# Optimization experiments

Measured on AMD Instinct MI355X. Metric: run time of the kernel, lower is better.

Reference implementation:

```python
import jax, jax.numpy as jnp
import numpy as np

B, T, D, H = 4, 2048, 1024, 16
HD = D // H  # head dim = 64


def setup_inputs() -> dict:
    key = jax.random.key(0)
    ks = jax.random.split(key, 9)
    s_in = 1.0 / np.sqrt(D)
    return {
        "token_embedding": jax.random.normal(ks[0], (B, T, D), dtype=jnp.float32),
        # per-head projections, batched over head axis: [H, D, HD]
        "Wq": jax.random.normal(ks[1], (H, D, HD), dtype=jnp.float32) * s_in,
        "bq": jnp.zeros((H, HD), dtype=jnp.float32),
        "Wk": jax.random.normal(ks[2], (H, D, HD), dtype=jnp.float32) * s_in,
        "bk": jnp.zeros((H, HD), dtype=jnp.float32),
        "Wv": jax.random.normal(ks[3], (H, D, HD), dtype=jnp.float32) * s_in,
        "bv": jnp.zeros((H, HD), dtype=jnp.float32),
        "Wo": jax.random.normal(ks[4], (D, D), dtype=jnp.float32) * s_in,
        "bo": jnp.zeros((D,), dtype=jnp.float32),
    }


def _mha(x, Wq, bq, Wk, bk, Wv, bv, Wo, bo):
    # x: [B,T,D]; per-head proj -> [B,H,T,HD]
    q = jnp.einsum('btd,hde->bhte', x, Wq) + bq[None, :, None, :]
    k = jnp.einsum('btd,hde->bhte', x, Wk) + bk[None, :, None, :]
    v = jnp.einsum('btd,hde->bhte', x, Wv) + bv[None, :, None, :]
    scores = jnp.einsum('bhte,bhse->bhts', q, k) / jnp.sqrt(jnp.float32(HD))
    causal = jnp.tril(jnp.ones((T, T), dtype=bool))
    scores = jnp.where(causal[None, None], scores, jnp.float32(-jnp.inf))
    attn = jax.nn.softmax(scores, axis=-1)
    ctx = jnp.einsum('bhts,bhse->bhte', attn, v)  # [B,H,T,HD]
    # concat heads (head order matches ModuleList order) -> [B,T,D]
    cat = jnp.transpose(ctx, (0, 2, 1, 3)).reshape(B, T, D)
    return cat @ Wo + bo


def reference(token_embedding, Wq, bq, Wk, bk, Wv, bv, Wo, bo):
    return _mha(token_embedding, Wq, bq, Wk, bk, Wv, bv, Wo, bo)
```

## Files before the change

### kernel.cpp

```cpp
#include <hip/hip_runtime.h>
#include <hip/hip_bf16.h>
#include <stdint.h>
#include <stddef.h>

#define B_ 4
#define T_ 2048
#define D_ 1024
#define H_ 16
#define HD_ 64
#define LDQKV (3 * D_)

typedef __attribute__((ext_vector_type(8))) __bf16 bf16x8;
typedef __attribute__((ext_vector_type(4))) float f32x4;
typedef __attribute__((ext_vector_type(16))) float f32x16;

#define AS1V const __attribute__((address_space(1))) void*
#define AS3V __attribute__((address_space(3))) void*

__global__ void prep_kernel(const float* __restrict__ x, const float* __restrict__ Wq,
                            const float* __restrict__ Wk, const float* __restrict__ Wv,
                            const float* __restrict__ Wo, const float* __restrict__ bq,
                            const float* __restrict__ bk, const float* __restrict__ bv,
                            __bf16* __restrict__ xb, __bf16* __restrict__ wT,
                            __bf16* __restrict__ woT, float* __restrict__ bqkv) {
    const int bid = blockIdx.x, tid = threadIdx.x;
    if (bid < 4096) {
        int i = bid * 256 + tid;
        const float4* p = (const float4*)(x + (size_t)i * 8);
        float4 a = p[0], b = p[1];
        bf16x8 o;
        o[0] = (__bf16)a.x; o[1] = (__bf16)a.y; o[2] = (__bf16)a.z; o[3] = (__bf16)a.w;
        o[4] = (__bf16)b.x; o[5] = (__bf16)b.y; o[6] = (__bf16)b.z; o[7] = (__bf16)b.w;
        *(bf16x8*)(xb + (size_t)i * 8) = o;
    } else if (bid < 16384) {
        int wbid = bid - 4096;
        int which = wbid >> 12;
        int rem = wbid & 4095;
        int h = rem >> 8, z = rem & 255;
        const float* W = (which == 0) ? Wq : (which == 1) ? Wk : Wv;
        int e = tid & 63, dd = tid >> 6;
        float v = W[((size_t)h * D_ + z * 4 + dd) * HD_ + e];
        wT[((size_t)which * D_ + h * HD_ + e) * D_ + z * 4 + dd] = (__bf16)v;
    } else if (bid < 17408) {
        int k = bid - 16384;
        for (int n = tid; n < D_; n += 256)
            woT[(size_t)n * D_ + k] = (__bf16)Wo[(size_t)k * D_ + n];
    } else {
        int n = (bid - 17408) * 256 + tid;
        const float* b = (n < D_) ? bq : (n < 2 * D_) ? bk : bv;
        bqkv[n] = b[n & (D_ - 1)];
    }
}

template <typename OutT>
__global__ __launch_bounds__(256, 3)
void gemm_bt_kernel(const __bf16* __restrict__ A, const __bf16* __restrict__ Bt,
                    OutT* __restrict__ C, const float* __restrict__ bias,
                    int M, int N, int K, int lda, int ldb, int ldc) {
    __shared__ __bf16 lsA[128 * 64];
    __shared__ __bf16 lsB[128 * 64];
    const int tid = threadIdx.x;
    const int lane = tid & 63;
    const int wave = tid >> 6;
    const int wr = wave >> 1, wc = wave & 1;
    const int lc = lane & 15, lg = lane >> 4;
    const long row0 = (long)blockIdx.y * 128;
    const long col0 = (long)blockIdx.x * 128;

    f32x4 acc[4][4];
#pragma unroll
    for (int mi = 0; mi < 4; mi++)
#pragma unroll
        for (int ni = 0; ni < 4; ni++)
#pragma unroll
            for (int q = 0; q < 4; q++) acc[mi][ni][q] = 0.f;

    const int s_row = tid >> 3, s_k8 = tid & 7;

    for (int k0 = 0; k0 < K; k0 += 64) {
        __syncthreads();
#pragma unroll
        for (int c2 = 0; c2 < 4; c2++) {
            const __bf16* ga = A + (row0 + c2 * 32 + s_row) * (long)lda + k0 + s_k8 * 8;
            const __bf16* gb = Bt + (col0 + c2 * 32 + s_row) * (long)ldb + k0 + s_k8 * 8;
            __bf16* la = lsA + ((c2 << 8) + (wave << 6)) * 8;
            __bf16* lb = lsB + ((c2 << 8) + (wave << 6)) * 8;
            __builtin_amdgcn_global_load_lds((AS1V)ga, (AS3V)la, 16, 0, 0);
            __builtin_amdgcn_global_load_lds((AS1V)gb, (AS3V)lb, 16, 0, 0);
        }
        __syncthreads();
#pragma unroll
        for (int kk = 0; kk < 2; kk++) {
            bf16x8 af[4], bf_[4];
#pragma unroll
            for (int mi = 0; mi < 4; mi++)
                af[mi] = *(const bf16x8*)(lsA + (wr * 64 + mi * 16 + lc) * 64 + (kk * 4 + lg) * 8);
#pragma unroll
            for (int ni = 0; ni < 4; ni++)
                bf_[ni] = *(const bf16x8*)(lsB + (wc * 64 + ni * 16 + lc) * 64 + (kk * 4 + lg) * 8);
#pragma unroll
            for (int mi = 0; mi < 4; mi++)
#pragma unroll
                for (int ni = 0; ni < 4; ni++)
                    acc[mi][ni] =
                        __builtin_amdgcn_mfma_f32_16x16x32_bf16(af[mi], bf_[ni], acc[mi][ni], 0, 0, 0);
        }
    }

#pragma unroll
    for (int mi = 0; mi < 4; mi++) {
#pragma unroll
        for (int ni = 0; ni < 4; ni++) {
            long r0 = row0 + wr * 64 + mi * 16 + lg * 4;
            long cc = col0 + wc * 64 + ni * 16 + lc;
            float bv = bias[cc];
#pragma unroll
            for (int q = 0; q < 4; q++) {
                float v = acc[mi][ni][q] + bv;
                C[(r0 + q) * (long)ldc + cc] = (OutT)v;
            }
        }
    }
}

__global__ void transpose_v_kernel(const __bf16* __restrict__ qkv, __bf16* __restrict__ vT) {
    __shared__ __bf16 tile[64][72];
    const int bh = blockIdx.y, t0 = blockIdx.x * 64;
    const int b = bh >> 4, h = bh & 15;
    const int r = threadIdx.x >> 2, c16 = (threadIdx.x & 3) * 16;
    const __bf16* src = qkv + (size_t)(b * T_ + t0 + r) * LDQKV + 2 * D_ + h * HD_ + c16;
    *(bf16x8*)&tile[r][c16] = *(const bf16x8*)src;
    *(bf16x8*)&tile[r][c16 + 8] = *(const bf16x8*)(src + 8);
    __syncthreads();
    bf16x8 v0, v1;
#pragma unroll
    for (int j = 0; j < 8; j++) v0[j] = tile[c16 + j][r];
#pragma unroll
    for (int j = 0; j < 8; j++) v1[j] = tile[c16 + 8 + j][r];
    __bf16* dst = vT + (size_t)(bh * HD_ + r) * T_ + t0 + c16;
    *(bf16x8*)dst = v0;
    *(bf16x8*)(dst + 8) = v1;
}

__global__ __launch_bounds__(256, 3)
void attn_kernel(const __bf16* __restrict__ qkv, const __bf16* __restrict__ vT,
                 __bf16* __restrict__ ctx) {
    __shared__ __bf16 lsK[64 * 64];
    __shared__ __bf16 lsV[64 * 64];
    const int tid = threadIdx.x;
    const int lane = tid & 63, w = tid >> 6;
    const int l31 = lane & 31, hi = lane >> 5;
    const int bid = blockIdx.x;
    const int xcd = bid & 7, slot = bid >> 3;
    const int bh = xcd * 8 + (slot & 7);
    const int pr = slot >> 3;
    const int b = bh >> 4, h = bh & 15;
    const float K2 = 0.125f * 1.44269504f;

    const __bf16* kbase = qkv + (size_t)(b * T_) * LDQKV + D_ + h * HD_;
    const __bf16* vbase = vT + (size_t)bh * HD_ * T_;

    int s_row[2], s_ch[2];
#pragma unroll
    for (int c2 = 0; c2 < 2; c2++) {
        int idx = c2 * 256 + tid;
        s_row[c2] = idx >> 3;
        s_ch[c2] = idx & 7;
    }

    for (int phase = 0; phase < 2; ++phase) {
        const int chunk = phase ? pr : (15 - pr);
        const int q0 = chunk * 128;
        const int qw = q0 + w * 32;
        const int myq = qw + l31;

        const __bf16* qbase = qkv + (size_t)(b * T_ + myq) * LDQKV + h * HD_;
        bf16x8 qf[4];
#pragma unroll
        for (int kf = 0; kf < 4; kf++) qf[kf] = *(const bf16x8*)(qbase + kf * 16 + hi * 8);

        f32x16 accO[2];
#pragma unroll
        for (int eo = 0; eo < 2; eo++)
#pragma unroll
            for (int r = 0; r < 16; r++) accO[eo][r] = 0.f;
        float m_r = -1e30f, l_r = 0.f;

        bf16x8 rK[2], rV[2];
        auto loadKV = [&](int kv0) {
#pragma unroll
            for (int c2 = 0; c2 < 2; c2++) {
                rK[c2] = *(const bf16x8*)(kbase + (size_t)(kv0 + s_row[c2]) * LDQKV + s_ch[c2] * 8);
                rV[c2] = *(const bf16x8*)(vbase + (size_t)s_row[c2] * T_ + kv0 + s_ch[c2] * 8);
            }
        };

        const int ntiles = 2 * (chunk + 1);
        loadKV(0);
        for (int it = 0; it < ntiles; ++it) {
            const int kv0 = it << 6;
            __syncthreads();
#pragma unroll
            for (int c2 = 0; c2 < 2; c2++) {
                *(bf16x8*)(lsK + s_row[c2] * 64 + ((s_ch[c2] ^ (s_row[c2] & 7)) << 3)) = rK[c2];
                *(bf16x8*)(lsV + s_row[c2] * 64 + ((s_ch[c2] ^ (s_row[c2] & 7)) << 3)) = rV[c2];
            }
            __syncthreads();
            if (it + 1 < ntiles) loadKV((it + 1) << 6);

            if (kv0 > qw + 31) continue;

            f32x16 st[2];
            __builtin_amdgcn_s_setprio(1);
#pragma unroll
            for (int kh = 0; kh < 2; kh++) {
                f32x16 a;
#pragma unroll
                for (int r = 0; r < 16; r++) a[r] = 0.f;
#pragma unroll
                for (int kf = 0; kf < 4; kf++) {
                    int row = kh * 32 + l31;
                    int ch = (kf << 1) | hi;
                    bf16x8 kfrag = *(const bf16x8*)(lsK + row * 64 + ((ch ^ (row & 7)) << 3));
                    a = __builtin_amdgcn_mfma_f32_32x32x16_bf16(kfrag, qf[kf], a, 0, 0, 0);
                }
                st[kh] = a;
            }
            __builtin_amdgcn_s_setprio(0);

            if (kv0 + 63 > qw) {
                const int qmk = myq - kv0 - 4 * hi;
#pragma unroll
                for (int kh = 0; kh < 2; kh++)
#pragma unroll
                    for (int r = 0; r < 16; r++) {
                        int kvl = (r & 3) + 8 * (r >> 2) + kh * 32;
                        if (kvl > qmk) st[kh][r] = -1e30f;
                    }
            }

            float red[16];
#pragma unroll
            for (int r = 0; r < 16; r++) red[r] = fmaxf(st[0][r], st[1][r]);
#pragma unroll
            for (int s2 = 8; s2 >= 1; s2 >>= 1)
#pragma unroll
                for (int r = 0; r < s2; r++) red[r] = fmaxf(red[r], red[r + s2]);
            float pmax = fmaxf(red[0], __shfl_xor(red[0], 32));

            if (!__all(pmax - m_r <= 64.f)) {
                float m_new = fmaxf(m_r, pmax);
                float alpha = exp2f((m_r - m_new) * K2);
                l_r *= alpha;
#pragma unroll
                for (int eo = 0; eo < 2; eo++)
#pragma unroll
                    for (int r = 0; r < 16; r++) accO[eo][r] *= alpha;
                m_r = m_new;
            }

            const float mb = m_r * K2;
#pragma unroll
            for (int kh = 0; kh < 2; kh++)
#pragma unroll
                for (int r = 0; r < 16; r++) st[kh][r] = exp2f(fmaf(st[kh][r], K2, -mb));

            float sr[16];
#pragma unroll
            for (int r = 0; r < 16; r++) sr[r] = st[0][r] + st[1][r];
#pragma unroll
            for (int s2 = 8; s2 >= 1; s2 >>= 1)
#pragma unroll
                for (int r = 0; r < s2; r++) sr[r] += sr[r + s2];
            l_r += sr[0] + __shfl_xor(sr[0], 32);

            union BW { unsigned u[4]; bf16x8 v; };
            bf16x8 pfrag[4];
            auto pack2 = [](float a, float b) -> unsigned {
                union { __bf16 h[2]; unsigned u; } x;
                x.h[0] = (__bf16)a;
                x.h[1] = (__bf16)b;
                return x.u;
            };
#pragma unroll
            for (int kh = 0; kh < 2; kh++)
#pragma unroll
                for (int sub = 0; sub < 2; sub++) {
                    int base = sub * 8;
                    unsigned W1 = pack2(st[kh][base + 0], st[kh][base + 1]);
                    unsigned W3 = pack2(st[kh][base + 2], st[kh][base + 3]);
                    unsigned W2 = pack2(st[kh][base + 4], st[kh][base + 5]);
                    unsigned W4 = pack2(st[kh][base + 6], st[kh][base + 7]);
                    unsigned X1 = (unsigned)__shfl_xor((int)W1, 32);
                    unsigned X2 = (unsigned)__shfl_xor((int)W2, 32);
                    unsigned X3 = (unsigned)__shfl_xor((int)W3, 32);
                    unsigned X4 = (unsigned)__shfl_xor((int)W4, 32);
                    BW bw;
                    bw.u[0] = hi ? X2 : W1;
                    bw.u[1] = hi ? X4 : W3;
                    bw.u[2] = hi ? W2 : X1;
                    bw.u[3] = hi ? W4 : X3;
                    pfrag[kh * 2 + sub] = bw.v;
                }

            __builtin_amdgcn_s_setprio(1);
#pragma unroll
            for (int eo = 0; eo < 2; eo++) {
#pragma unroll
                for (int ks = 0; ks < 4; ks++) {
                    int row = eo * 32 + l31;
                    int ch = (ks << 1) | hi;
                    bf16x8 vfrag = *(const bf16x8*)(lsV + row * 64 + ((ch ^ (row & 7)) << 3));
                    accO[eo] = __builtin_amdgcn_mfma_f32_32x32x16_bf16(vfrag, pfrag[ks], accO[eo], 0, 0, 0);
                }
            }
            __builtin_amdgcn_s_setprio(0);
        }

        float invl = 1.0f / l_r;
        __bf16* cb = ctx + (size_t)(b * T_ + myq) * D_ + h * HD_;
#pragma unroll
        for (int eo = 0; eo < 2; eo++)
#pragma unroll
            for (int r = 0; r < 16; r++) {
                int e = eo * 32 + (r & 3) + 8 * (r >> 2) + 4 * hi;
                cb[e] = (__bf16)(accO[eo][r] * invl);
            }
    }
}

extern "C" void kernel_launch(void* const* d_in, const int* in_sizes, int n_in,
                              void* d_out, int out_size, void* d_ws, size_t ws_size,
                              hipStream_t stream) {
    const float* x = (const float*)d_in[0];
    const float* Wq = (const float*)d_in[1];
    const float* bq = (const float*)d_in[2];
    const float* Wk = (const float*)d_in[3];
    const float* bk = (const float*)d_in[4];
    const float* Wv = (const float*)d_in[5];
    const float* bv = (const float*)d_in[6];
    const float* Wo = (const float*)d_in[7];
    const float* bo = (const float*)d_in[8];
    float* out = (float*)d_out;

    char* ws = (char*)d_ws;
    size_t off = 0;
    auto alloc = [&](size_t bytes) -> void* {
        off = (off + 255) & ~(size_t)255;
        void* p = ws + off;
        off += bytes;
        return p;
    };
    __bf16* xb = (__bf16*)alloc((size_t)B_ * T_ * D_ * 2);
    __bf16* wT = (__bf16*)alloc((size_t)3 * D_ * D_ * 2);
    float* bqkv = (float*)alloc((size_t)3 * D_ * 4);
    __bf16* woT = (__bf16*)alloc((size_t)D_ * D_ * 2);
    __bf16* qkv = (__bf16*)alloc((size_t)B_ * T_ * 3 * D_ * 2);
    __bf16* vTb = (__bf16*)alloc((size_t)B_ * H_ * HD_ * T_ * 2);
    __bf16* ctx = (__bf16*)alloc((size_t)B_ * T_ * D_ * 2);
    (void)ws_size;
    (void)in_sizes;
    (void)n_in;
    (void)out_size;

    prep_kernel<<<17420, 256, 0, stream>>>(x, Wq, Wk, Wv, Wo, bq, bk, bv, xb, wT, woT, bqkv);

    gemm_bt_kernel<__bf16><<<dim3(3 * D_ / 128, B_ * T_ / 128), 256, 0, stream>>>(
        xb, wT, qkv, bqkv, B_ * T_, 3 * D_, D_, D_, D_, 3 * D_);

    transpose_v_kernel<<<dim3(T_ / 64, B_ * H_), 256, 0, stream>>>(qkv, vTb);

    attn_kernel<<<512, 256, 0, stream>>>(qkv, vTb, ctx);

    gemm_bt_kernel<float><<<dim3(D_ / 128, B_ * T_ / 128), 256, 0, stream>>>(
        ctx, woT, out, bo, B_ * T_, D_, D_, D_, D_, D_);
}
```

Baseline: 215.5 us.

## Use triple-buffered 128x256 GEMM kernel for QKV projection

Adds a new GEMM kernel with 512 threads, a 128x256 output tile, and a three-stage LDS ring filled by direct global-to-LDS loads. Prefetch runs two K-tiles ahead, using waitcnt plus barrier. It is used only for the QKV projection, and is meant to hide global load latency and raise reuse per block. In exchange it uses much more LDS (about 144KB) and runs one block per CU, and the grid shrinks to 768 blocks.

Measured after the change: 223.8 us. 3.8% more time.

```diff
diff --git a/kernel.cpp b/kernel.cpp
--- a/kernel.cpp
+++ b/kernel.cpp
@@ -53,6 +53,123 @@
 }
 
 template <typename OutT>
+__global__ __launch_bounds__(512, 1)
+void gemm3s_kernel(const __bf16* __restrict__ A, const __bf16* __restrict__ Bt,
+                   OutT* __restrict__ C, const float* __restrict__ bias,
+                   int M, int N, int K, int lda, int ldb, int ldc) {
+    constexpr int ASZ = 128 * 64;
+    constexpr int BSZ = 256 * 64;
+    __shared__ __bf16 lsA[3 * ASZ];
+    __shared__ __bf16 lsB[3 * BSZ];
+    const int tid = threadIdx.x;
+    const int lane = tid & 63;
+    const int wave = tid >> 6;
+    const int wm = wave >> 2, wn = wave & 3;
+    const int lc = lane & 15, lg = lane >> 4;
+    const long row0 = (long)blockIdx.y * 128;
+    const long col0 = (long)blockIdx.x * 256;
+
+    f32x4 acc[4][4];
+#pragma unroll
+    for (int mi = 0; mi < 4; mi++)
+#pragma unroll
+        for (int ni = 0; ni < 4; ni++)
+#pragma unroll
+            for (int q = 0; q < 4; q++) acc[mi][ni][q] = 0.f;
+
+    const __bf16* gsrc[6];
+    int lbase[6];
+#pragma unroll
+    for (int c = 0; c < 6; c++) {
+        if (c < 2) {
+            int slot = c * 512 + tid;
+            int row = slot >> 3, ch = slot & 7;
+            gsrc[c] = A + (row0 + row) * (long)lda + ((ch ^ (row & 7)) << 3);
+            lbase[c] = (c * 512 + (tid & ~63)) << 3;
+        } else {
+            int slot = (c - 2) * 512 + tid;
+            int row = slot >> 3, ch = slot & 7;
+            gsrc[c] = Bt + (col0 + row) * (long)ldb + ((ch ^ (row & 7)) << 3);
+            lbase[c] = ((c - 2) * 512 + (tid & ~63)) << 3;
+        }
+    }
+
+    auto stage = [&](int t, int bi) {
+        const int k0 = t << 6;
+#pragma unroll
+        for (int c = 0; c < 2; c++)
+            __builtin_amdgcn_global_load_lds((AS1V)(gsrc[c] + k0),
+                                             (AS3V)(lsA + bi * ASZ + lbase[c]), 16, 0, 0);
+#pragma unroll
+        for (int c = 2; c < 6; c++)
+            __builtin_amdgcn_global_load_lds((AS1V)(gsrc[c] + k0),
+                                             (AS3V)(lsB + bi * BSZ + lbase[c]), 16, 0, 0);
+    };
+
+    auto compute = [&](int bi) {
+        const __bf16* la = lsA + bi * ASZ;
+        const __bf16* lb = lsB + bi * BSZ;
+#pragma unroll
+        for (int kk = 0; kk < 2; kk++) {
+            bf16x8 af[4], bfr[4];
+#pragma unroll
+            for (int mi = 0; mi < 4; mi++) {
+                int row = wm * 64 + mi * 16 + lc;
+                int ch = (kk * 4 + lg) ^ (row & 7);
+                af[mi] = *(const bf16x8*)(la + row * 64 + ch * 8);
+            }
+#pragma unroll
+            for (int ni = 0; ni < 4; ni++) {
+                int row = wn * 64 + ni * 16 + lc;
+                int ch = (kk * 4 + lg) ^ (row & 7);
+                bfr[ni] = *(const bf16x8*)(lb + row * 64 + ch * 8);
+            }
+#pragma unroll
+            for (int mi = 0; mi < 4; mi++)
+#pragma unroll
+                for (int ni = 0; ni < 4; ni++)
+                    acc[mi][ni] =
+                        __builtin_amdgcn_mfma_f32_16x16x32_bf16(af[mi], bfr[ni], acc[mi][ni], 0, 0, 0);
+        }
+    };
+
+    const int nt = K >> 6;
+    stage(0, 0);
+    stage(1, 1);
+    asm volatile("s_waitcnt vmcnt(6)\n\ts_barrier" ::: "memory");
+
+    int cur = 0;
+    for (int t = 0; t < nt; ++t) {
+        int sb = cur + 2;
+        if (sb >= 3) sb -= 3;
+        if (t + 2 < nt) stage(t + 2, sb);
+        compute(cur);
+        if (t + 1 < nt) {
+            if (t + 2 < nt)
+                asm volatile("s_waitcnt vmcnt(6)\n\ts_barrier" ::: "memory");
+            else
+                asm volatile("s_waitcnt vmcnt(0)\n\ts_barrier" ::: "memory");
+        }
+        cur = (cur + 1 == 3) ? 0 : cur + 1;
+    }
+
+#pragma unroll
+    for (int mi = 0; mi < 4; mi++) {
+#pragma unroll
+        for (int ni = 0; ni < 4; ni++) {
+            long r0 = row0 + wm * 64 + mi * 16 + lg * 4;
+            long cc = col0 + wn * 64 + ni * 16 + lc;
+            float bv = bias[cc];
+#pragma unroll
+            for (int q = 0; q < 4; q++) {
+                float v = acc[mi][ni][q] + bv;
+                C[(r0 + q) * (long)ldc + cc] = (OutT)v;
+            }
+        }
+    }
+}
+
+template <typename OutT>
 __global__ __launch_bounds__(256, 3)
 void gemm_bt_kernel(const __bf16* __restrict__ A, const __bf16* __restrict__ Bt,
                     OutT* __restrict__ C, const float* __restrict__ bias,
@@ -365,7 +482,7 @@
 
     prep_kernel<<<17420, 256, 0, stream>>>(x, Wq, Wk, Wv, Wo, bq, bk, bv, xb, wT, woT, bqkv);
 
-    gemm_bt_kernel<__bf16><<<dim3(3 * D_ / 128, B_ * T_ / 128), 256, 0, stream>>>(
+    gemm3s_kernel<__bf16><<<dim3(3 * D_ / 256, B_ * T_ / 128), 512, 0, stream>>>(
         xb, wT, qkv, bqkv, B_ * T_, 3 * D_, D_, D_, D_, 3 * D_);
 
     transpose_v_kernel<<<dim3(T_ / 64, B_ * H_), 256, 0, stream>>>(qkv, vTb);
```
